# Optimization experiments

Measured on AMD Instinct MI355X. Metric: run time of the kernel, lower is better.

## Reference

```python
import jax, jax.numpy as jnp
import numpy as np

N_NODES = 100000
N_EDGES = 1600000
HIDDEN = 128
N_LAYERS = 3
N_GRAPHS = 100
EPS = 1e-5


def setup_inputs() -> dict:
    key = jax.random.key(0)
    ks = jax.random.split(key, 9)
    node = jax.random.normal(ks[0], (N_NODES, HIDDEN), dtype=jnp.float32)
    edge_index = jax.random.randint(ks[1], (2, N_EDGES), 0, N_NODES, dtype=jnp.int32)
    edge_attr = jax.random.uniform(ks[2], (N_EDGES,), dtype=jnp.float32)
    batch_ptr = jnp.sort(jax.random.randint(ks[3], (N_NODES,), 0, N_GRAPHS, dtype=jnp.int32))
    W = jax.random.normal(ks[4], (N_LAYERS, HIDDEN, HIDDEN), dtype=jnp.float32) * (1.0 / np.sqrt(HIDDEN))
    b = jax.random.normal(ks[5], (N_LAYERS, HIDDEN), dtype=jnp.float32) * 0.02
    gn_weight = jnp.ones((N_LAYERS, HIDDEN), dtype=jnp.float32)
    gn_bias = jnp.zeros((N_LAYERS, HIDDEN), dtype=jnp.float32)
    gn_alpha = jnp.ones((N_LAYERS, HIDDEN), dtype=jnp.float32)
    return {"node": node, "edge_index": edge_index, "edge_attr": edge_attr,
            "batch_ptr": batch_ptr, "W": W, "b": b, "gn_weight": gn_weight,
            "gn_bias": gn_bias, "gn_alpha": gn_alpha}


def reference(node, edge_index, edge_attr, batch_ptr, W, b, gn_weight, gn_bias, gn_alpha):
    N, d = node.shape
    src, dst = edge_index[0], edge_index[1]
    # GCN normalization with self-loops (weight 1), as in PyG gcn_norm
    loop = jnp.arange(N, dtype=src.dtype)
    src_a = jnp.concatenate([src, loop])
    dst_a = jnp.concatenate([dst, loop])
    w_a = jnp.concatenate([edge_attr, jnp.ones((N,), dtype=edge_attr.dtype)])
    deg = jax.ops.segment_sum(w_a, dst_a, num_segments=N)
    dis = jnp.where(deg > 0, deg ** -0.5, 0.0)
    norm = dis[src_a] * w_a * dis[dst_a]  # [E+N]

    counts = jax.ops.segment_sum(jnp.ones((N,), node.dtype), batch_ptr,
                                 num_segments=N_GRAPHS)[:, None]  # [G,1]

    for l in range(W.shape[0]):
        # GCNConv: linear transform, then gather-normalize-scatter over edges
        h = node @ W[l]  # [N,d]
        agg = jax.ops.segment_sum(norm[:, None] * h[src_a], dst_a, num_segments=N) + b[l]
        # GraphNorm: per-graph mean shift (scaled by alpha) and variance norm
        mean = jax.ops.segment_sum(agg, batch_ptr, num_segments=N_GRAPHS) / counts  # [G,d]
        sub = agg - gn_alpha[l] * mean[batch_ptr]
        var = jax.ops.segment_sum(sub * sub, batch_ptr, num_segments=N_GRAPHS) / counts
        node = jax.nn.relu(gn_weight[l] * sub * jax.lax.rsqrt(var[batch_ptr] + EPS) + gn_bias[l])
    return node
```

## Files before the change

kernel.cpp:

```cpp
#include <hip/hip_runtime.h>
#include <cstdint>

#define N_N 100000
#define N_E 1600000
#define HID 128
#define N_G 100
#define EPSF 1e-5f

static inline int ceil_div(int a, int b){ return (a + b - 1) / b; }

typedef __attribute__((ext_vector_type(8))) short bf16x8;
typedef __attribute__((ext_vector_type(4))) float f32x4;

__device__ inline float bf2f(unsigned short u){
  return __uint_as_float(((unsigned int)u) << 16);
}
__device__ inline unsigned short f2bf(float f){
  unsigned int u = __float_as_uint(f);
  unsigned int r = u + 0x7fffu + ((u >> 16) & 1u);
  return (unsigned short)(r >> 16);
}
__device__ inline void fma8(float* acc, float nv, uint4 u){
  acc[0] += nv * __uint_as_float(u.x << 16);
  acc[1] += nv * __uint_as_float(u.x & 0xffff0000u);
  acc[2] += nv * __uint_as_float(u.y << 16);
  acc[3] += nv * __uint_as_float(u.y & 0xffff0000u);
  acc[4] += nv * __uint_as_float(u.z << 16);
  acc[5] += nv * __uint_as_float(u.z & 0xffff0000u);
  acc[6] += nv * __uint_as_float(u.w << 16);
  acc[7] += nv * __uint_as_float(u.w & 0xffff0000u);
}


__global__ void k_init(int* __restrict__ degi, float* __restrict__ counts){
  int i = blockIdx.x * 256 + threadIdx.x;
  if (i < N_N) degi[i] = 0;
  if (i < N_G) counts[i] = 0.0f;
}

__global__ void k_cnt(const int* __restrict__ dst, int* __restrict__ degi,
                      int* __restrict__ rank){
  int e = blockIdx.x * 256 + threadIdx.x;
  if (e < N_E) rank[e] = atomicAdd(&degi[dst[e]], 1);
}

__global__ void k_counts(const int* __restrict__ bp, float* __restrict__ counts){
  int t = blockIdx.x * 256 + threadIdx.x;
  int r0 = t * 32;
  if (r0 >= N_N) return;
  int r1 = min(r0 + 32, N_N);
  int curg = bp[r0];
  float acc = 0.f;
  for (int r = r0; r < r1; ++r){
    int g = bp[r];
    if (g != curg){ atomicAdd(&counts[curg], acc); acc = 0.f; curg = g; }
    acc += 1.0f;
  }
  atomicAdd(&counts[curg], acc);
}


__global__ __launch_bounds__(256) void k_scanA(const int* __restrict__ degi,
                                               int* __restrict__ partial,
                                               int* __restrict__ bsum){
  __shared__ int s[256];
  int t = threadIdx.x;
  int i = blockIdx.x * 256 + t;
  int v = (i < N_N) ? degi[i] : 0;
  s[t] = v; __syncthreads();
  #pragma unroll
  for (int off = 1; off < 256; off <<= 1){
    int tmp = (t >= off) ? s[t - off] : 0;
    __syncthreads();
    s[t] += tmp;
    __syncthreads();
  }
  if (i < N_N) partial[i] = s[t] - v;
  if (t == 255) bsum[blockIdx.x] = s[255];
}

__global__ __launch_bounds__(512) void k_scanB(int* __restrict__ bsum, int nblocks){
  __shared__ int s[512];
  int t = threadIdx.x;
  int v = (t < nblocks) ? bsum[t] : 0;
  s[t] = v; __syncthreads();
  #pragma unroll
  for (int off = 1; off < 512; off <<= 1){
    int tmp = (t >= off) ? s[t - off] : 0;
    __syncthreads();
    s[t] += tmp;
    __syncthreads();
  }
  if (t < nblocks) bsum[t] = s[t] - v;
}

__global__ void k_scanC(const int* __restrict__ partial, const int* __restrict__ bsum,
                        int* __restrict__ ptr){
  int i = blockIdx.x * 256 + threadIdx.x;
  if (i < N_N) ptr[i] = partial[i] + bsum[blockIdx.x];
  if (i == 0) ptr[N_N] = N_E;
}

__global__ void k_fill(const int* __restrict__ src, const int* __restrict__ dst,
                       const float* __restrict__ w, const int* __restrict__ rank,
                       const int* __restrict__ ptr, int2* __restrict__ edge8){
  int e = blockIdx.x * 256 + threadIdx.x;
  if (e < N_E){
    int d = dst[e];
    int slot = ptr[d] + rank[e];
    edge8[slot] = make_int2(src[e], __float_as_int(w[e]));
  }
}

__global__ void k_dis(const int* __restrict__ ptr, const int2* __restrict__ edge8,
                      float* __restrict__ dis, float* __restrict__ nself){
  int i = blockIdx.x * 256 + threadIdx.x;
  if (i >= N_N) return;
  int e0 = ptr[i], e1 = ptr[i + 1];
  float d = 1.0f;
  for (int e = e0; e < e1; ++e) d += __int_as_float(edge8[e].y);
  float r = d > 0.f ? rsqrtf(d) : 0.f;
  dis[i] = r;
  nself[i] = r * r;
}

__global__ void k_ne(const int* __restrict__ ptr, const float* __restrict__ dis,
                     int2* __restrict__ edge8){
  int i = blockIdx.x * 256 + threadIdx.x;
  if (i >= N_N) return;
  float di = dis[i];
  int e0 = ptr[i], e1 = ptr[i + 1];
  for (int e = e0; e < e1; ++e){
    int2 v = edge8[e];
    float ne = dis[v.x] * __int_as_float(v.y) * di;
    ((float*)&edge8[e])[1] = ne;
  }
}

__global__ void k_wt(const float* __restrict__ W, unsigned short* __restrict__ Wt){
  int i = blockIdx.x * 256 + threadIdx.x;
  if (i >= HID * HID) return;
  int n = i >> 7, k = i & 127;
  Wt[i] = f2bf(W[k * HID + n]);
}

__global__ __launch_bounds__(256) void k_gemm(const float* __restrict__ X,
                                              const float* __restrict__ agg,
                                              int fused,
                                              const int* __restrict__ bp,
                                              const float* __restrict__ mean,
                                              const float* __restrict__ rstd,
                                              const float* __restrict__ alpha,
                                              const float* __restrict__ gwv,
                                              const float* __restrict__ gbv,
                                              const unsigned short* __restrict__ Wt,
                                              unsigned short* __restrict__ Hb, int nrows){
  __shared__ unsigned short lA[64 * 136];
  __shared__ unsigned short lB[128 * 136];
  int tid = threadIdx.x;
  int row0 = blockIdx.x * 64;

  #pragma unroll
  for (int i = 0; i < 8; ++i){
    int c = tid + i * 256;
    int r = c >> 4, cc = c & 15;
    *(uint4*)&lB[r * 136 + cc * 8] = ((const uint4*)Wt)[c];
  }
  #pragma unroll
  for (int i = 0; i < 8; ++i){
    int c = tid + i * 256;
    int r = c >> 5, cc = c & 31;
    int gr = row0 + r;
    float4 v = make_float4(0.f, 0.f, 0.f, 0.f);
    if (gr < nrows){
      if (!fused){
        v = *(const float4*)(X + (size_t)gr * HID + cc * 4);
      } else {
        int g = bp[gr];
        float4 a  = *(const float4*)(agg  + (size_t)gr * HID + cc * 4);
        float4 m  = *(const float4*)(mean + g * HID + cc * 4);
        float4 rs = *(const float4*)(rstd + g * HID + cc * 4);
        float4 al = *(const float4*)(alpha + cc * 4);
        float4 wv = *(const float4*)(gwv + cc * 4);
        float4 bv = *(const float4*)(gbv + cc * 4);
        v.x = fmaxf(wv.x * (a.x - al.x * m.x) * rs.x + bv.x, 0.f);
        v.y = fmaxf(wv.y * (a.y - al.y * m.y) * rs.y + bv.y, 0.f);
        v.z = fmaxf(wv.z * (a.z - al.z * m.z) * rs.z + bv.z, 0.f);
        v.w = fmaxf(wv.w * (a.w - al.w * m.w) * rs.w + bv.w, 0.f);
      }
    }
    unsigned short pk[4] = {f2bf(v.x), f2bf(v.y), f2bf(v.z), f2bf(v.w)};
    *(uint2*)&lA[r * 136 + cc * 4] = *(const uint2*)pk;
  }
  __syncthreads();

  int wave = tid >> 6;
  int lane = tid & 63;
  int l16 = lane & 15;
  int quad = lane >> 4;
  int am = wave * 16 + l16;

  bf16x8 afr[4];
  #pragma unroll
  for (int kc = 0; kc < 4; ++kc)
    afr[kc] = *(const bf16x8*)&lA[am * 136 + kc * 32 + quad * 8];

  #pragma unroll
  for (int nt = 0; nt < 8; ++nt){
    f32x4 acc = {0.f, 0.f, 0.f, 0.f};
    int bn = nt * 16 + l16;
    #pragma unroll
    for (int kc = 0; kc < 4; ++kc){
      bf16x8 bfr = *(const bf16x8*)&lB[bn * 136 + kc * 32 + quad * 8];
      acc = __builtin_amdgcn_mfma_f32_16x16x32_bf16(afr[kc], bfr, acc, 0, 0, 0);
    }
    int gr = row0 + wave * 16 + quad * 4;
    #pragma unroll
    for (int r = 0; r < 4; ++r){
      if (gr + r < nrows)
        Hb[(size_t)(gr + r) * HID + nt * 16 + l16] = f2bf(acc[r]);
    }
  }
}

__global__ __launch_bounds__(256) void k_gather(const int* __restrict__ ptr,
                                                const int2* __restrict__ edge8,
                                                const unsigned short* __restrict__ Hb,
                                                const float* __restrict__ nself,
                                                const float* __restrict__ bias,
                                                float* __restrict__ agg){
  int t = blockIdx.x * 256 + threadIdx.x;
  int node = t >> 4;
  if (node >= N_N) return;
  int lane = t & 15;
  const uint4* h16 = (const uint4*)Hb;
  float ns = nself[node];
  uint4 hu = h16[(size_t)node * 16 + lane];
  float4 b0 = ((const float4*)bias)[lane * 2];
  float4 b1 = ((const float4*)bias)[lane * 2 + 1];
  float acc[8] = {b0.x, b0.y, b0.z, b0.w, b1.x, b1.y, b1.z, b1.w};
  fma8(acc, ns, hu);

  int e0 = ptr[node], e1 = ptr[node + 1];
  int e = e0;
  for (; e + 4 <= e1; e += 4){
    int2 ev0 = edge8[e + 0];
    int2 ev1 = edge8[e + 1];
    int2 ev2 = edge8[e + 2];
    int2 ev3 = edge8[e + 3];
    uint4 r0 = h16[(size_t)ev0.x * 16 + lane];
    uint4 r1 = h16[(size_t)ev1.x * 16 + lane];
    uint4 r2 = h16[(size_t)ev2.x * 16 + lane];
    uint4 r3 = h16[(size_t)ev3.x * 16 + lane];
    fma8(acc, __int_as_float(ev0.y), r0);
    fma8(acc, __int_as_float(ev1.y), r1);
    fma8(acc, __int_as_float(ev2.y), r2);
    fma8(acc, __int_as_float(ev3.y), r3);
  }
  for (; e < e1; ++e){
    int2 ev = edge8[e];
    uint4 r0 = h16[(size_t)ev.x * 16 + lane];
    fma8(acc, __int_as_float(ev.y), r0);
  }
  float4* ap = (float4*)(agg + (size_t)node * HID + lane * 8);
  ap[0] = make_float4(acc[0], acc[1], acc[2], acc[3]);
  ap[1] = make_float4(acc[4], acc[5], acc[6], acc[7]);
}


__global__ void k_zero2(float* __restrict__ a, float* __restrict__ b){
  int i = blockIdx.x * 256 + threadIdx.x;
  if (i < N_G * HID){ a[i] = 0.f; b[i] = 0.f; }
}

__global__ __launch_bounds__(128) void k_gstat(const float* __restrict__ agg,
                                               const int* __restrict__ bp,
                                               float* __restrict__ sum,
                                               float* __restrict__ sumsq){
  int f = threadIdx.x;
  int r0 = blockIdx.x * 64;
  int r1 = min(r0 + 64, N_N);
  int curg = bp[r0];
  float s = 0.f, s2 = 0.f;
  for (int r = r0; r < r1; ++r){
    int g = bp[r];
    if (g != curg){
      atomicAdd(&sum[curg * HID + f], s);
      atomicAdd(&sumsq[curg * HID + f], s2);
      s = 0.f; s2 = 0.f; curg = g;
    }
    float v = agg[(size_t)r * HID + f];
    s += v; s2 += v * v;
  }
  atomicAdd(&sum[curg * HID + f], s);
  atomicAdd(&sumsq[curg * HID + f], s2);
}

__global__ void k_finstat(const float* __restrict__ sum, const float* __restrict__ sumsq,
                          const float* __restrict__ counts, const float* __restrict__ alpha,
                          float* __restrict__ mean, float* __restrict__ rstd){
  int i = blockIdx.x * 256 + threadIdx.x;
  if (i >= N_G * HID) return;
  int f = i & (HID - 1);
  float c = counts[i >> 7];
  float inv = c > 0.f ? 1.0f / c : 0.f;
  float m = sum[i] * inv;
  float ex2 = sumsq[i] * inv;
  float al = alpha[f];
  float var = ex2 - m * m * al * (2.0f - al);
  mean[i] = m;
  rstd[i] = rsqrtf(var + EPSF);
}

__global__ void k_out(const float* __restrict__ agg, const int* __restrict__ bp,
                      const float* __restrict__ mean, const float* __restrict__ rstd,
                      const float* __restrict__ alpha, const float* __restrict__ gw,
                      const float* __restrict__ gb, float* __restrict__ out){
  int idx = blockIdx.x * 256 + threadIdx.x;
  if (idx >= N_N * 32) return;
  int i = idx >> 5, q = idx & 31;
  int g = bp[i];
  float4 a  = ((const float4*)agg)[idx];
  float4 m  = ((const float4*)mean)[g * 32 + q];
  float4 r  = ((const float4*)rstd)[g * 32 + q];
  float4 al = ((const float4*)alpha)[q];
  float4 wv = ((const float4*)gw)[q];
  float4 bv = ((const float4*)gb)[q];
  float4 o;
  o.x = fmaxf(wv.x * (a.x - al.x * m.x) * r.x + bv.x, 0.f);
  o.y = fmaxf(wv.y * (a.y - al.y * m.y) * r.y + bv.y, 0.f);
  o.z = fmaxf(wv.z * (a.z - al.z * m.z) * r.z + bv.z, 0.f);
  o.w = fmaxf(wv.w * (a.w - al.w * m.w) * r.w + bv.w, 0.f);
  ((float4*)out)[idx] = o;
}


extern "C" void kernel_launch(void* const* d_in, const int* in_sizes, int n_in,
                              void* d_out, int out_size, void* d_ws, size_t ws_size,
                              hipStream_t stream){
  const float* node0 = (const float*)d_in[0];
  const int*   eidx  = (const int*)d_in[1];
  const float* eattr = (const float*)d_in[2];
  const int*   bp    = (const int*)d_in[3];
  const float* W     = (const float*)d_in[4];
  const float* bias  = (const float*)d_in[5];
  const float* gw    = (const float*)d_in[6];
  const float* gb    = (const float*)d_in[7];
  const float* ga    = (const float*)d_in[8];
  float* out = (float*)d_out;
  const int* src = eidx;
  const int* dst = eidx + N_E;

  char* p = (char*)d_ws;
  auto carve = [&](size_t nbytes) -> char* {
    char* q = p; p += (nbytes + 255) & ~(size_t)255; return q;
  };
  float* dis    = (float*)carve((size_t)N_N * 4);
  float* nself  = (float*)carve((size_t)N_N * 4);
  float* counts = (float*)carve((size_t)N_G * 4);
  int*   degi   = (int*)  carve((size_t)N_N * 4);
  int*   partial= (int*)  carve((size_t)N_N * 4);
  int*   bsum   = (int*)  carve((size_t)512 * 4);
  int*   ptr    = (int*)  carve((size_t)(N_N + 1) * 4);
  int*   rank   = (int*)  carve((size_t)N_E * 4);
  int2*  edge8  = (int2*) carve((size_t)N_E * 8);
  unsigned short* hb = (unsigned short*)carve((size_t)N_N * HID * 2);
  unsigned short* wt = (unsigned short*)carve((size_t)HID * HID * 2);
  float* agg    = (float*)carve((size_t)N_N * HID * 4);
  float* mean   = (float*)carve((size_t)N_G * HID * 4);
  float* rstd   = (float*)carve((size_t)N_G * HID * 4);
  float* sum    = (float*)carve((size_t)N_G * HID * 4);
  float* sumsq  = (float*)carve((size_t)N_G * HID * 4);

  int nblocks = ceil_div(N_N, 256);

  k_init  <<<nblocks, 256, 0, stream>>>(degi, counts);
  k_cnt   <<<ceil_div(N_E, 256), 256, 0, stream>>>(dst, degi, rank);
  k_counts<<<ceil_div(N_N, 32 * 256), 256, 0, stream>>>(bp, counts);
  k_scanA <<<nblocks, 256, 0, stream>>>(degi, partial, bsum);
  k_scanB <<<1, 512, 0, stream>>>(bsum, nblocks);
  k_scanC <<<nblocks, 256, 0, stream>>>(partial, bsum, ptr);
  k_fill  <<<ceil_div(N_E, 256), 256, 0, stream>>>(src, dst, eattr, rank, ptr, edge8);
  k_dis   <<<nblocks, 256, 0, stream>>>(ptr, edge8, dis, nself);
  k_ne    <<<nblocks, 256, 0, stream>>>(ptr, dis, edge8);

  for (int l = 0; l < 3; ++l){
    k_wt <<<ceil_div(HID * HID, 256), 256, 0, stream>>>(W + (size_t)l * HID * HID, wt);
    if (l == 0){
      k_gemm <<<ceil_div(N_N, 64), 256, 0, stream>>>(node0, nullptr, 0,
                 nullptr, nullptr, nullptr, nullptr, nullptr, nullptr, wt, hb, N_N);
    } else {
      k_gemm <<<ceil_div(N_N, 64), 256, 0, stream>>>(nullptr, agg, 1,
                 bp, mean, rstd, ga + (l - 1) * HID, gw + (l - 1) * HID,
                 gb + (l - 1) * HID, wt, hb, N_N);
    }
    k_gather <<<ceil_div(N_N * 16, 256), 256, 0, stream>>>(ptr, edge8, hb, nself,
                 bias + l * HID, agg);
    k_zero2  <<<ceil_div(N_G * HID, 256), 256, 0, stream>>>(sum, sumsq);
    k_gstat  <<<ceil_div(N_N, 64), 128, 0, stream>>>(agg, bp, sum, sumsq);
    k_finstat<<<ceil_div(N_G * HID, 256), 256, 0, stream>>>(sum, sumsq, counts,
                 ga + l * HID, mean, rstd);
  }
  k_out <<<ceil_div(N_N * 32, 256), 256, 0, stream>>>(agg, bp, mean, rstd,
             ga + 2 * HID, gw + 2 * HID, gb + 2 * HID, out);
}
```

Measured before the change: 649.2 us.

## Build CSR with two-level bucketed counting sort and batch weight conversion

Replaces the global-atomic degree count and rank-based scatter with a two-pass bucket sort. Edges are first histogrammed and partitioned into 256-node buckets using shared-memory atomics, then each bucket is locally sorted into CSR while degree and normalization are computed in the same pass. The three per-layer weight transposes are merged into one launch. The change aims to cut contended global atomics and random scatter writes, at the cost of an intermediate partition buffer (aliased onto agg) and packing the local dst index into the upper bits of src.

Result: faster. 591.9 us (-8.8%).

```diff
diff --git a/kernel.cpp b/kernel.cpp
--- a/kernel.cpp
+++ b/kernel.cpp
@@ -6,6 +6,10 @@
 #define HID 128
 #define N_G 100
 #define EPSF 1e-5f
+
+#define NB   256
+#define EPB  ((N_E + NB - 1) / NB)
+#define NBKT ((N_N + 255) >> 8)
 
 static inline int ceil_div(int a, int b){ return (a + b - 1) / b; }
 
@@ -31,17 +35,15 @@
   acc[7] += nv * __uint_as_float(u.w & 0xffff0000u);
 }
 
-
-__global__ void k_init(int* __restrict__ degi, float* __restrict__ counts){
+__global__ void k_wt3(const float* __restrict__ W, unsigned short* __restrict__ Wt,
+                      float* __restrict__ counts){
   int i = blockIdx.x * 256 + threadIdx.x;
-  if (i < N_N) degi[i] = 0;
   if (i < N_G) counts[i] = 0.0f;
-}
-
-__global__ void k_cnt(const int* __restrict__ dst, int* __restrict__ degi,
-                      int* __restrict__ rank){
-  int e = blockIdx.x * 256 + threadIdx.x;
-  if (e < N_E) rank[e] = atomicAdd(&degi[dst[e]], 1);
+  if (i >= 3 * HID * HID) return;
+  int l = i >> 14;
+  int r = i & 16383;
+  int n = r >> 7, k = r & 127;
+  Wt[i] = f2bf(W[l * HID * HID + k * HID + n]);
 }
 
 __global__ void k_counts(const int* __restrict__ bp, float* __restrict__ counts){
@@ -59,14 +61,25 @@
   atomicAdd(&counts[curg], acc);
 }
 
-
-__global__ __launch_bounds__(256) void k_scanA(const int* __restrict__ degi,
-                                               int* __restrict__ partial,
-                                               int* __restrict__ bsum){
+__global__ __launch_bounds__(256) void k_hist(const int* __restrict__ dst,
+                                              int* __restrict__ counts){
+  __shared__ int h[NBKT];
+  int t = threadIdx.x, blk = blockIdx.x;
+  for (int i = t; i < NBKT; i += 256) h[i] = 0;
+  __syncthreads();
+  int e0 = blk * EPB, e1 = min(e0 + EPB, N_E);
+  for (int e = e0 + t; e < e1; e += 256)
+    atomicAdd(&h[dst[e] >> 8], 1);
+  __syncthreads();
+  for (int i = t; i < NBKT; i += 256) counts[i * NB + blk] = h[i];
+}
+
+__global__ __launch_bounds__(256) void k_scanA(int* __restrict__ data,
+                                               int* __restrict__ bsum, int n){
   __shared__ int s[256];
   int t = threadIdx.x;
   int i = blockIdx.x * 256 + t;
-  int v = (i < N_N) ? degi[i] : 0;
+  int v = (i < n) ? data[i] : 0;
   s[t] = v; __syncthreads();
   #pragma unroll
   for (int off = 1; off < 256; off <<= 1){
@@ -75,7 +88,7 @@
     s[t] += tmp;
     __syncthreads();
   }
-  if (i < N_N) partial[i] = s[t] - v;
+  if (i < n) data[i] = s[t] - v;
   if (t == 255) bsum[blockIdx.x] = s[255];
 }
 
@@ -94,34 +107,77 @@
   if (t < nblocks) bsum[t] = s[t] - v;
 }
 
-__global__ void k_scanC(const int* __restrict__ partial, const int* __restrict__ bsum,
-                        int* __restrict__ ptr){
+__global__ void k_scanC(int* __restrict__ data, const int* __restrict__ bsum, int n){
   int i = blockIdx.x * 256 + threadIdx.x;
-  if (i < N_N) ptr[i] = partial[i] + bsum[blockIdx.x];
-  if (i == 0) ptr[N_N] = N_E;
-}
-
-__global__ void k_fill(const int* __restrict__ src, const int* __restrict__ dst,
-                       const float* __restrict__ w, const int* __restrict__ rank,
-                       const int* __restrict__ ptr, int2* __restrict__ edge8){
-  int e = blockIdx.x * 256 + threadIdx.x;
-  if (e < N_E){
+  if (i < n) data[i] += bsum[blockIdx.x];
+}
+
+__global__ __launch_bounds__(256) void k_part(const int* __restrict__ src,
+                                              const int* __restrict__ dst,
+                                              const float* __restrict__ w,
+                                              const int* __restrict__ coff,
+                                              int2* __restrict__ part){
+  __shared__ int off[NBKT];
+  int t = threadIdx.x, blk = blockIdx.x;
+  for (int i = t; i < NBKT; i += 256) off[i] = coff[i * NB + blk];
+  __syncthreads();
+  int e0 = blk * EPB, e1 = min(e0 + EPB, N_E);
+  for (int e = e0 + t; e < e1; e += 256){
     int d = dst[e];
-    int slot = ptr[d] + rank[e];
-    edge8[slot] = make_int2(src[e], __float_as_int(w[e]));
-  }
-}
-
-__global__ void k_dis(const int* __restrict__ ptr, const int2* __restrict__ edge8,
-                      float* __restrict__ dis, float* __restrict__ nself){
-  int i = blockIdx.x * 256 + threadIdx.x;
-  if (i >= N_N) return;
-  int e0 = ptr[i], e1 = ptr[i + 1];
-  float d = 1.0f;
-  for (int e = e0; e < e1; ++e) d += __int_as_float(edge8[e].y);
-  float r = d > 0.f ? rsqrtf(d) : 0.f;
-  dis[i] = r;
-  nself[i] = r * r;
+    int pos = atomicAdd(&off[d >> 8], 1);
+    part[pos] = make_int2(src[e] | ((d & 255) << 24), __float_as_int(w[e]));
+  }
+}
+
+__global__ __launch_bounds__(256) void k_csr(const int* __restrict__ coff,
+                                             const int2* __restrict__ part,
+                                             int2* __restrict__ edge8,
+                                             int* __restrict__ ptr,
+                                             float* __restrict__ dis,
+                                             float* __restrict__ nself){
+  __shared__ int h[256];
+  __shared__ int c[256];
+  __shared__ float wsum[256];
+  __shared__ int s[256];
+  int t = threadIdx.x, b = blockIdx.x;
+  int base  = coff[b * NB];
+  int base2 = (b + 1 < NBKT) ? coff[(b + 1) * NB] : N_E;
+  h[t] = 0; c[t] = 0; wsum[t] = 0.f;
+  __syncthreads();
+  for (int e = base + t; e < base2; e += 256){
+    int2 v = part[e];
+    int local = ((unsigned int)v.x) >> 24;
+    atomicAdd(&h[local], 1);
+    atomicAdd(&wsum[local], __int_as_float(v.y));
+  }
+  __syncthreads();
+  int v0 = h[t];
+  s[t] = v0; __syncthreads();
+  #pragma unroll
+  for (int off = 1; off < 256; off <<= 1){
+    int tmp = (t >= off) ? s[t - off] : 0;
+    __syncthreads();
+    s[t] += tmp;
+    __syncthreads();
+  }
+  int mybase = base + s[t] - v0;
+  int node = (b << 8) + t;
+  if (node < N_N){
+    ptr[node] = mybase;
+    float d = 1.0f + wsum[t];
+    float r = rsqrtf(d);
+    dis[node] = r;
+    nself[node] = r * r;
+  }
+  if (b == NBKT - 1 && t == 0) ptr[N_N] = N_E;
+  h[t] = mybase;
+  __syncthreads();
+  for (int e = base + t; e < base2; e += 256){
+    int2 v = part[e];
+    int local = ((unsigned int)v.x) >> 24;
+    int pos = h[local] + atomicAdd(&c[local], 1);
+    edge8[pos] = make_int2(v.x & 0x00ffffff, v.y);
+  }
 }
 
 __global__ void k_ne(const int* __restrict__ ptr, const float* __restrict__ dis,
@@ -135,13 +191,6 @@
     float ne = dis[v.x] * __int_as_float(v.y) * di;
     ((float*)&edge8[e])[1] = ne;
   }
-}
-
-__global__ void k_wt(const float* __restrict__ W, unsigned short* __restrict__ Wt){
-  int i = blockIdx.x * 256 + threadIdx.x;
-  if (i >= HID * HID) return;
-  int n = i >> 7, k = i & 127;
-  Wt[i] = f2bf(W[k * HID + n]);
 }
 
 __global__ __launch_bounds__(256) void k_gemm(const float* __restrict__ X,
@@ -358,41 +407,43 @@
   float* dis    = (float*)carve((size_t)N_N * 4);
   float* nself  = (float*)carve((size_t)N_N * 4);
   float* counts = (float*)carve((size_t)N_G * 4);
-  int*   degi   = (int*)  carve((size_t)N_N * 4);
-  int*   partial= (int*)  carve((size_t)N_N * 4);
+  int*   coff   = (int*)  carve((size_t)NBKT * NB * 4);
   int*   bsum   = (int*)  carve((size_t)512 * 4);
   int*   ptr    = (int*)  carve((size_t)(N_N + 1) * 4);
-  int*   rank   = (int*)  carve((size_t)N_E * 4);
   int2*  edge8  = (int2*) carve((size_t)N_E * 8);
   unsigned short* hb = (unsigned short*)carve((size_t)N_N * HID * 2);
-  unsigned short* wt = (unsigned short*)carve((size_t)HID * HID * 2);
+  unsigned short* wt = (unsigned short*)carve((size_t)3 * HID * HID * 2);
   float* agg    = (float*)carve((size_t)N_N * HID * 4);
   float* mean   = (float*)carve((size_t)N_G * HID * 4);
   float* rstd   = (float*)carve((size_t)N_G * HID * 4);
   float* sum    = (float*)carve((size_t)N_G * HID * 4);
   float* sumsq  = (float*)carve((size_t)N_G * HID * 4);
-
-  int nblocks = ceil_div(N_N, 256);
-
-  k_init  <<<nblocks, 256, 0, stream>>>(degi, counts);
-  k_cnt   <<<ceil_div(N_E, 256), 256, 0, stream>>>(dst, degi, rank);
+  int2*  part   = (int2*)agg;
+
+  int nscan = NBKT * NB;
+  int nscan_blocks = ceil_div(nscan, 256);
+
+  k_wt3   <<<ceil_div(3 * HID * HID, 256), 256, 0, stream>>>(W, wt, counts);
   k_counts<<<ceil_div(N_N, 32 * 256), 256, 0, stream>>>(bp, counts);
-  k_scanA <<<nblocks, 256, 0, stream>>>(degi, partial, bsum);
-  k_scanB <<<1, 512, 0, stream>>>(bsum, nblocks);
-  k_scanC <<<nblocks, 256, 0, stream>>>(partial, bsum, ptr);
-  k_fill  <<<ceil_div(N_E, 256), 256, 0, stream>>>(src, dst, eattr, rank, ptr, edge8);
-  k_dis   <<<nblocks, 256, 0, stream>>>(ptr, edge8, dis, nself);
-  k_ne    <<<nblocks, 256, 0, stream>>>(ptr, dis, edge8);
+  k_hist  <<<NB, 256, 0, stream>>>(dst, coff);
+  k_scanA <<<nscan_blocks, 256, 0, stream>>>(coff, bsum, nscan);
+  k_scanB <<<1, 512, 0, stream>>>(bsum, nscan_blocks);
+  k_scanC <<<nscan_blocks, 256, 0, stream>>>(coff, bsum, nscan);
+  k_part  <<<NB, 256, 0, stream>>>(src, dst, eattr, coff, part);
+  k_csr   <<<NBKT, 256, 0, stream>>>(coff, part, edge8, ptr, dis, nself);
+  k_ne    <<<ceil_div(N_N, 256), 256, 0, stream>>>(ptr, dis, edge8);
 
   for (int l = 0; l < 3; ++l){
-    k_wt <<<ceil_div(HID * HID, 256), 256, 0, stream>>>(W + (size_t)l * HID * HID, wt);
     if (l == 0){
       k_gemm <<<ceil_div(N_N, 64), 256, 0, stream>>>(node0, nullptr, 0,
-                 nullptr, nullptr, nullptr, nullptr, nullptr, nullptr, wt, hb, N_N);
+                 nullptr, nullptr, nullptr, nullptr, nullptr, nullptr,
+                 wt, hb, N_N);
     } else {
       k_gemm <<<ceil_div(N_N, 64), 256, 0, stream>>>(nullptr, agg, 1,
                  bp, mean, rstd, ga + (l - 1) * HID, gw + (l - 1) * HID,
-                 gb + (l - 1) * HID, wt, hb, N_N);
+                 gb + (l - 1) * HID, wt + (size_t)l * HID * HID, hb, N_N);
+    }
+    if (l == 0){
     }
     k_gather <<<ceil_div(N_N * 16, 256), 256, 0, stream>>>(ptr, edge8, hb, nself,
                  bias + l * HID, agg);
```
